# Kernel tuning notes

Measured on AMD Instinct MI355X. Metric: run time of the kernel, lower is better.

Reference implementation:

```python
import jax, jax.numpy as jnp
import numpy as np

XD, D, R, MIXN = 8, 64, 64, 32
BATCH, SEQ = 2048, 128
EPS = 1e-5
LOG2PI = float(np.log(2.0 * np.pi))


def softsign(x):
    return x / (1.0 + jnp.abs(x))


def batchnorm(x, gamma, beta):
    # BatchNorm1d in training mode: per-call batch statistics (biased var)
    mu = jnp.mean(x, axis=0)
    var = jnp.var(x, axis=0)
    return gamma * (x - mu) * jax.lax.rsqrt(var + EPS) + beta


def setup_inputs() -> dict:
    key = jax.random.key(0)
    ks = jax.random.split(key, 20)
    def lin(k, out_d, in_d):
        bound = 1.0 / np.sqrt(in_d)
        k1, k2 = jax.random.split(k)
        W = jax.random.uniform(k1, (out_d, in_d), minval=-bound, maxval=bound, dtype=jnp.float32)
        b = jax.random.uniform(k2, (out_d,), minval=-bound, maxval=bound, dtype=jnp.float32)
        return W, b
    X = jax.random.normal(ks[0], (BATCH, XD, SEQ), dtype=jnp.float32)
    enc_w, enc_b = lin(ks[1], D, XD)
    init_w = jax.random.normal(ks[2], (1, R), dtype=jnp.float32)
    A = jax.random.normal(ks[3], (R, D, R), dtype=jnp.float32)
    muW, mub = lin(ks[4], MIXN * XD, R)
    muW2, mub2 = lin(ks[5], MIXN * XD, MIXN * XD)
    sigW, sigb = lin(ks[6], MIXN * XD, R)
    sigW2, sigb2 = lin(ks[7], MIXN * XD, MIXN * XD)
    alW, alb = lin(ks[8], MIXN, R)
    alW2, alb2 = lin(ks[9], MIXN, MIXN)
    bn_g = jnp.ones((R,), jnp.float32)
    bn_b = jnp.zeros((R,), jnp.float32)
    return dict(X=X, enc_w=enc_w, enc_b=enc_b, init_w=init_w, A=A, bn_g=bn_g, bn_b=bn_b,
                muW=muW, mub=mub, muW2=muW2, mub2=mub2, sigW=sigW, sigb=sigb,
                sigW2=sigW2, sigb2=sigb2, alW=alW, alb=alb, alW2=alW2, alb2=alb2)


def reference(X, enc_w, enc_b, init_w, A, bn_g, bn_b,
              muW, mub, muW2, mub2, sigW, sigb, sigW2, sigb2,
              alW, alb, alW2, alb2):
    B, _, L = X.shape

    def phi(x, tmp):
        # GMM log-likelihood head; h = softmax of hidden state
        h = jax.nn.softmax(tmp, axis=1)                       # [B, R]
        mu = softsign(h @ muW.T + mub) @ muW2.T + mub2        # [B, MIXN*XD]
        logsig = softsign(h @ sigW.T + sigb) @ sigW2.T + sigb2
        log_alpha = jax.nn.log_softmax(
            softsign(h @ alW.T + alb) @ alW2.T + alb2, axis=1)  # [B, MIXN]
        mu = mu.reshape(B, MIXN, XD)
        logsig = logsig.reshape(B, MIXN, XD)
        sig = jnp.exp(logsig)
        z = (x[:, None, :] - mu) / sig
        comp_lp = jnp.sum(-0.5 * z * z - logsig - 0.5 * LOG2PI, axis=-1)  # [B, MIXN]
        return jax.scipy.special.logsumexp(log_alpha + comp_lp, axis=1)  # [B]

    # step 0: broadcast initial weight
    tmp0 = batchnorm(jnp.tile(init_w, (B, 1)), bn_g, bn_b)
    res0 = phi(X[:, :, 0], tmp0)
    norm0 = jnp.sum(tmp0 * tmp0)

    x_prev = jnp.moveaxis(X[:, :, :L - 1], 2, 0)  # [L-1, B, XD]
    x_cur = jnp.moveaxis(X[:, :, 1:], 2, 0)       # [L-1, B, XD]

    def step(carry, inputs):
        tmp, res, norm = carry
        xp, xc = inputs
        enc = softsign(xp @ enc_w.T + enc_b)                 # encoding()
        new = jnp.einsum('nd,ni,idj->nj', enc, tmp, A)       # trilinear transition
        new = batchnorm(new, bn_g, bn_b)
        res = res + phi(xc, new)
        norm = norm + jnp.sum(new * new)
        return (new, res, norm), None

    (_, res, norm), _ = jax.lax.scan(step, (tmp0, res0, norm0), (x_prev, x_cur))
    return res, norm
```

## Files before the change

### kernel.cpp

```cpp
#include <hip/hip_runtime.h>

typedef unsigned short u16;
typedef short short8 __attribute__((ext_vector_type(8)));
typedef float f32x4 __attribute__((ext_vector_type(4)));
typedef unsigned uint4v __attribute__((ext_vector_type(4)));

#define LOG2PI_HALF 0.91893853320467274f
#define AO __ATOMIC_RELAXED
#define AS __HIP_MEMORY_SCOPE_AGENT

static constexpr size_t OFF_STATS = 0;
static constexpr size_t OFF_NEW   = 65536;
static constexpr size_t OFF_AT    = OFF_NEW + (size_t)128*2048*64*2;
static constexpr size_t OFF_MUW   = OFF_AT   + (size_t)64*4096*2;
static constexpr size_t OFF_SIGW  = OFF_MUW  + (size_t)256*64*2;
static constexpr size_t OFF_ALW   = OFF_SIGW + (size_t)256*64*2;
static constexpr size_t OFF_MUW2  = OFF_ALW  + (size_t)32*64*2;
static constexpr size_t OFF_SIGW2 = OFF_MUW2 + (size_t)256*256*2;
static constexpr size_t OFF_ALW2  = OFF_SIGW2+ (size_t)256*256*2;
static constexpr size_t OFF_CNT   = OFF_ALW2 + (size_t)32*32*2;
static constexpr size_t OFF_PART  = OFF_CNT + 1024;
static constexpr size_t WS_NEED   = OFF_PART + (size_t)2*128*128*4;

static __device__ __forceinline__ u16 f2bf(float x) {
  unsigned u = __builtin_bit_cast(unsigned, x);
  u += 0x7fffu + ((u >> 16) & 1u);
  return (u16)(u >> 16);
}
static __device__ __forceinline__ float bf2f(u16 b) {
  unsigned u = ((unsigned)b) << 16;
  return __builtin_bit_cast(float, u);
}
static __device__ __forceinline__ unsigned pk2(float a, float b) {
  return ((unsigned)f2bf(b) << 16) | (unsigned)f2bf(a);
}

__global__ void init_kernel(
    const float* __restrict__ A, const float* __restrict__ init_w,
    const float* __restrict__ muW, const float* __restrict__ sigW, const float* __restrict__ alW,
    const float* __restrict__ muW2, const float* __restrict__ sigW2, const float* __restrict__ alW2,
    u16* __restrict__ At, u16* __restrict__ new0, float* __restrict__ stats0,
    u16* __restrict__ muWb, u16* __restrict__ sigWb, u16* __restrict__ alWb,
    u16* __restrict__ muW2b, u16* __restrict__ sigW2b, u16* __restrict__ alW2b)
{
  const int total = 560192;
  for (int idx = blockIdx.x*256 + threadIdx.x; idx < total; idx += gridDim.x*256) {
    if (idx < 262144) {
      int j = idx >> 12, k = idx & 4095;
      At[idx] = f2bf(A[k*64 + j]);
    } else if (idx < 393216) {
      int e = idx - 262144;
      new0[e] = f2bf(init_w[e & 63]);
    } else if (idx < 409600) { int e = idx - 393216; muWb[e]   = f2bf(muW[e]);
    } else if (idx < 425984) { int e = idx - 409600; sigWb[e]  = f2bf(sigW[e]);
    } else if (idx < 428032) { int e = idx - 425984; alWb[e]   = f2bf(alW[e]);
    } else if (idx < 493568) { int e = idx - 428032; muW2b[e]  = f2bf(muW2[e]);
    } else if (idx < 559104) { int e = idx - 493568; sigW2b[e] = f2bf(sigW2[e]);
    } else if (idx < 560128) { int e = idx - 559104; alW2b[e]  = f2bf(alW2[e]);
    } else {
      int e = idx - 560128;
      float wv = bf2f(f2bf(init_w[e]));
      stats0[e]      = 2048.0f * wv;
      stats0[64 + e] = 2048.0f * (wv * wv);
    }
  }
}

struct ChainS {
  float newf[16][64];
  float tmp_s[16][66];
  float enc_s[16][68];
  float xp_s[16][8];
  float ab_s[2][64];
  float psum[4][128];
  float red_s[8][16][64];
  float sred[2][16][66];
};
struct PhiS {
  u16 h_s[32][72];
  u16 smu[32][264];
  u16 ssg[32][264];
  u16 sal[32][40];
  float xc_s[32][8];
  float clp_s[32][32];
  float alo_s[32][34];
  float bias_s[1088];
  float ab2[2][64];
};
union SmemU { ChainS c; PhiS p; };

__global__ __launch_bounds__(512) void fused_kernel(
    u16* __restrict__ newa, float* stats, int* flags, float* part,
    const float* __restrict__ X,
    const float* __restrict__ enc_w, const float* __restrict__ enc_b,
    const float* __restrict__ bn_g, const float* __restrict__ bn_b,
    const u16* __restrict__ At, const float* __restrict__ init_w,
    const u16* __restrict__ muWb, const u16* __restrict__ sigWb, const u16* __restrict__ alWb,
    const u16* __restrict__ muW2b, const u16* __restrict__ sigW2b, const u16* __restrict__ alW2b,
    const float* __restrict__ mub, const float* __restrict__ sigb, const float* __restrict__ alb,
    const float* __restrict__ mub2, const float* __restrict__ sigb2, const float* __restrict__ alb2,
    float* __restrict__ outp)
{
  __shared__ SmemU smem;
  const int tid = threadIdx.x;
  const int bid = blockIdx.x;
  const int lane = tid & 63, w = tid >> 6;
  const int m = lane & 15, q = lane >> 4;
  int* sflag = flags + 128;

  if (bid < 128) {
    const int n0 = bid * 16;
    for (int e = tid; e < 1024; e += 512) {
      int r = e >> 6, c0 = e & 63;
      smem.c.newf[r][c0] = bf2f(f2bf(init_w[c0]));
    }

    for (int t = 1; t < 128; ++t) {
      if (tid < 128) {
        int r = tid >> 3, k = tid & 7;
        smem.c.xp_s[r][k] = X[(size_t)(n0+r)*1024 + k*128 + (t-1)];
      }
      __syncthreads();
      {
        int r = tid >> 5, d0 = (tid & 31) * 2;
        #pragma unroll
        for (int dd = 0; dd < 2; ++dd) {
          int d = d0 + dd;
          float a = enc_b[d];
          #pragma unroll
          for (int k = 0; k < 8; ++k) a = fmaf(smem.c.xp_s[r][k], enc_w[d*8+k], a);
          smem.c.enc_s[r][d] = a / (1.0f + fabsf(a));
        }
      }

      if (t >= 2) {
        if (w == 0) {
          for (;;) {
            int v0 = __hip_atomic_load(flags + lane*2,     AO, AS);
            int v1 = __hip_atomic_load(flags + lane*2 + 1, AO, AS);
            if (__ballot((v0 >= t-1) && (v1 >= t-1)) == ~0ull) break;
            __builtin_amdgcn_s_sleep(1);
          }
        }
        __syncthreads();
        __atomic_signal_fence(__ATOMIC_ACQUIRE);
        {
          const int e = tid & 127, pr = tid >> 7;
          const float* pb = part + (size_t)((t-1)&1)*16384 + e;
          float s = 0.0f;
          #pragma unroll 16
          for (int p = pr*32; p < pr*32 + 32; ++p)
            s += __hip_atomic_load(pb + p*128, AO, AS);
          smem.c.psum[pr][e] = s;
        }
        __syncthreads();
        if (bid == 0 && tid < 128) {
          float sv = smem.c.psum[0][tid] + smem.c.psum[1][tid] + smem.c.psum[2][tid] + smem.c.psum[3][tid];
          __hip_atomic_store(stats + (t-1)*128 + tid, sv, AO, AS);
        }
        if (tid < 64) {
          float S1 = smem.c.psum[0][tid] + smem.c.psum[1][tid] + smem.c.psum[2][tid] + smem.c.psum[3][tid];
          float S2 = smem.c.psum[0][tid+64] + smem.c.psum[1][tid+64] + smem.c.psum[2][tid+64] + smem.c.psum[3][tid+64];
          float mean = S1 * (1.0f/2048.0f);
          float var  = S2 * (1.0f/2048.0f) - mean*mean;
          float a = bn_g[tid] * rsqrtf(var + 1e-5f);
          smem.c.ab_s[0][tid] = a;
          smem.c.ab_s[1][tid] = fmaf(-a, mean, bn_b[tid]);
        }
      } else {
        if (tid < 64) {
          float mean = bf2f(f2bf(init_w[tid]));
          float a = bn_g[tid] * rsqrtf(1e-5f);
          smem.c.ab_s[0][tid] = a;
          smem.c.ab_s[1][tid] = fmaf(-a, mean, bn_b[tid]);
        }
      }
      __syncthreads();
      if (bid == 0 && tid == 0 && t >= 2)
        __hip_atomic_store(sflag, t-1, AO, AS);

      #pragma unroll
      for (int e0 = 0; e0 < 1024; e0 += 512) {
        int e = e0 + tid;
        int mr = e >> 6, i = e & 63;
        smem.c.tmp_s[mr][i] = fmaf(smem.c.ab_s[0][i], smem.c.newf[mr][i], smem.c.ab_s[1][i]);
      }
      __syncthreads();

      f32x4 acc[4];
      #pragma unroll
      for (int nt = 0; nt < 4; ++nt) acc[nt] = 0;

      #pragma unroll 4
      for (int it = 0; it < 16; ++it) {
        const int k0 = w*512 + it*32;
        const int i = k0 >> 6;
        const int dbase = (k0 & 63) + q*8;
        const float tv = smem.c.tmp_s[m][i];
        const f32x4 e0 = *reinterpret_cast<const f32x4*>(&smem.c.enc_s[m][dbase]);
        const f32x4 e1 = *reinterpret_cast<const f32x4*>(&smem.c.enc_s[m][dbase+4]);
        uint4v pk;
        pk[0] = pk2(tv*e0[0], tv*e0[1]);
        pk[1] = pk2(tv*e0[2], tv*e0[3]);
        pk[2] = pk2(tv*e1[0], tv*e1[1]);
        pk[3] = pk2(tv*e1[2], tv*e1[3]);
        short8 af = __builtin_bit_cast(short8, pk);
        const u16* bp = At + k0 + q*8;
        #pragma unroll
        for (int nt = 0; nt < 4; ++nt) {
          short8 bfv = *reinterpret_cast<const short8*>(bp + (nt*16 + m)*4096);
          acc[nt] = __builtin_amdgcn_mfma_f32_16x16x32_bf16(af, bfv, acc[nt], 0, 0, 0);
        }
      }
      #pragma unroll
      for (int nt = 0; nt < 4; ++nt)
        #pragma unroll
        for (int rg = 0; rg < 4; ++rg)
          smem.c.red_s[w][q*4+rg][nt*16+m] = acc[nt][rg];
      __syncthreads();

      {
        u16* no = newa + (size_t)t*2048*64;
        const int r = tid >> 5;
        const int c2 = (tid & 31) * 2;
        float v0 = 0.0f, v1 = 0.0f;
        #pragma unroll
        for (int p = 0; p < 8; ++p) { v0 += smem.c.red_s[p][r][c2]; v1 += smem.c.red_s[p][r][c2+1]; }
        smem.c.newf[r][c2]   = v0;
        smem.c.newf[r][c2+1] = v1;
        __hip_atomic_store((unsigned*)(no + (size_t)(n0+r)*64 + c2), pk2(v0, v1), AO, AS);
        smem.c.sred[0][r][c2]   = v0;  smem.c.sred[0][r][c2+1] = v1;
        smem.c.sred[1][r][c2]   = v0*v0; smem.c.sred[1][r][c2+1] = v1*v1;
      }
      __syncthreads();
      if (tid < 64) {
        float S1 = 0.0f, S2 = 0.0f;
        #pragma unroll
        for (int r = 0; r < 16; ++r) { S1 += smem.c.sred[0][r][tid]; S2 += smem.c.sred[1][r][tid]; }
        float* pb = part + (size_t)(t&1)*16384 + bid*128;
        __hip_atomic_store(pb + tid,      S1, AO, AS);
        __hip_atomic_store(pb + 64 + tid, S2, AO, AS);
      }
      __syncthreads();
      if (tid == 0)
        __hip_atomic_store(flags + bid, t, AO, AS);
    }

    if (bid == 0) {
      if (w == 0) {
        for (;;) {
          int v0 = __hip_atomic_load(flags + lane*2,     AO, AS);
          int v1 = __hip_atomic_load(flags + lane*2 + 1, AO, AS);
          if (__ballot((v0 >= 127) && (v1 >= 127)) == ~0ull) break;
          __builtin_amdgcn_s_sleep(1);
        }
      }
      __syncthreads();
      __atomic_signal_fence(__ATOMIC_ACQUIRE);
      {
        const int e = tid & 127, pr = tid >> 7;
        const float* pb = part + (size_t)(127&1)*16384 + e;
        float s = 0.0f;
        #pragma unroll 16
        for (int p = pr*32; p < pr*32 + 32; ++p)
          s += __hip_atomic_load(pb + p*128, AO, AS);
        smem.c.psum[pr][e] = s;
      }
      __syncthreads();
      if (tid < 128) {
        float sv = smem.c.psum[0][tid] + smem.c.psum[1][tid] + smem.c.psum[2][tid] + smem.c.psum[3][tid];
        __hip_atomic_store(stats + 127*128 + tid, sv, AO, AS);
      }
      __syncthreads();
      if (tid == 0) __hip_atomic_store(sflag, 127, AO, AS);
    }

  } else {
    const int cc  = bid - 128;
    const int n0p = (cc & 63) * 32;
    const int par = cc >> 6;
    const int r32 = tid >> 4;
    const int x16 = tid & 15;

    for (int e = tid; e < 1088; e += 512) {
      float v;
      if      (e < 256)  v = mub[e];
      else if (e < 512)  v = sigb[e-256];
      else if (e < 544)  v = alb[e-512];
      else if (e < 800)  v = mub2[e-544];
      else if (e < 1056) v = sigb2[e-800];
      else               v = alb2[e-1056];
      smem.p.bias_s[e] = v;
    }
    float nrm_acc = 0.0f;

    for (int kk = 0; kk < 64; ++kk) {
      const int t = 2*kk + par;
      if (t > 0 && tid == 0) {
        while (__hip_atomic_load(sflag, AO, AS) < t)
          __builtin_amdgcn_s_sleep(1);
      }
      __syncthreads();
      __atomic_signal_fence(__ATOMIC_ACQUIRE);
      if (tid < 64) {
        float s1 = __hip_atomic_load(stats + t*128 + tid,      AO, AS);
        float s2 = __hip_atomic_load(stats + t*128 + 64 + tid, AO, AS);
        float mean = s1 * (1.0f/2048.0f);
        float var  = s2 * (1.0f/2048.0f) - mean*mean;
        float a = bn_g[tid] * rsqrtf(var + 1e-5f);
        smem.p.ab2[0][tid] = a;
        smem.p.ab2[1][tid] = fmaf(-a, mean, bn_b[tid]);
      }
      __syncthreads();

      {
        const u16* na = newa + (size_t)t*2048*64 + (size_t)(n0p + r32)*64 + x16*4;
        unsigned d0 = __hip_atomic_load((const unsigned*)na,     AO, AS);
        unsigned d1 = __hip_atomic_load((const unsigned*)na + 1, AO, AS);
        const int ib = x16*4;
        float tv[4];
        tv[0] = fmaf(smem.p.ab2[0][ib],   bf2f((u16)(d0 & 0xffff)), smem.p.ab2[1][ib]);
        tv[1] = fmaf(smem.p.ab2[0][ib+1], bf2f((u16)(d0 >> 16)),    smem.p.ab2[1][ib+1]);
        tv[2] = fmaf(smem.p.ab2[0][ib+2], bf2f((u16)(d1 & 0xffff)), smem.p.ab2[1][ib+2]);
        tv[3] = fmaf(smem.p.ab2[0][ib+3], bf2f((u16)(d1 >> 16)),    smem.p.ab2[1][ib+3]);
        float nacc = 0.0f, mx = -3.4e38f;
        #pragma unroll
        for (int j = 0; j < 4; ++j) { nacc = fmaf(tv[j], tv[j], nacc); mx = fmaxf(mx, tv[j]); }
        mx = fmaxf(mx, __shfl_xor(mx, 1));
        mx = fmaxf(mx, __shfl_xor(mx, 2));
        mx = fmaxf(mx, __shfl_xor(mx, 4));
        mx = fmaxf(mx, __shfl_xor(mx, 8));
        float se = 0.0f;
        #pragma unroll
        for (int j = 0; j < 4; ++j) { tv[j] = __expf(tv[j] - mx); se += tv[j]; }
        se += __shfl_xor(se, 1);
        se += __shfl_xor(se, 2);
        se += __shfl_xor(se, 4);
        se += __shfl_xor(se, 8);
        float inv = 1.0f / se;
        #pragma unroll
        for (int j = 0; j < 4; ++j) smem.p.h_s[r32][ib + j] = f2bf(tv[j] * inv);
        nacc += __shfl_xor(nacc, 1);
        nacc += __shfl_xor(nacc, 2);
        nacc += __shfl_xor(nacc, 4);
        nacc += __shfl_xor(nacc, 8);
        nacc += __shfl_xor(nacc, 16);
        nacc += __shfl_xor(nacc, 32);
        nrm_acc += nacc;
        if (x16 < 8) smem.p.xc_s[r32][x16] = X[(size_t)(n0p+r32)*1024 + x16*128 + t];
      }
      __syncthreads();

      {
        const u16* W1 = (w < 4) ? muWb : sigWb;
        const int boff = (w < 4) ? 0 : 256;
        const int coloff = (w & 3) * 64;
        f32x4 acc2[2][4];
        #pragma unroll
        for (int a_ = 0; a_ < 2; ++a_)
          #pragma unroll
          for (int b_ = 0; b_ < 4; ++b_) acc2[a_][b_] = 0;
        #pragma unroll
        for (int mt = 0; mt < 2; ++mt)
          #pragma unroll
          for (int kit = 0; kit < 2; ++kit) {
            short8 af = *reinterpret_cast<const short8*>(&smem.p.h_s[mt*16+m][kit*32 + q*8]);
            #pragma unroll
            for (int nt = 0; nt < 4; ++nt) {
              int c_ = coloff + nt*16 + m;
              short8 bfv = *reinterpret_cast<const short8*>(W1 + c_*64 + kit*32 + q*8);
              acc2[mt][nt] = __builtin_amdgcn_mfma_f32_16x16x32_bf16(af, bfv, acc2[mt][nt], 0, 0, 0);
            }
          }
        #pragma unroll
        for (int mt = 0; mt < 2; ++mt)
          #pragma unroll
          for (int nt = 0; nt < 4; ++nt) {
            int col = coloff + nt*16 + m;
            float bia = smem.p.bias_s[boff + col];
            #pragma unroll
            for (int rg = 0; rg < 4; ++rg) {
              int row = mt*16 + q*4 + rg;
              float v = acc2[mt][nt][rg] + bia;
              v = v / (1.0f + fabsf(v));
              ((w < 4) ? smem.p.smu : smem.p.ssg)[row][col] = f2bf(v);
            }
          }
      }
      if (w == 0) {
        f32x4 aacc[2][2];
        aacc[0][0] = 0; aacc[0][1] = 0; aacc[1][0] = 0; aacc[1][1] = 0;
        #pragma unroll
        for (int mt = 0; mt < 2; ++mt)
          #pragma unroll
          for (int kit = 0; kit < 2; ++kit) {
            short8 af = *reinterpret_cast<const short8*>(&smem.p.h_s[mt*16+m][kit*32 + q*8]);
            #pragma unroll
            for (int nt = 0; nt < 2; ++nt) {
              short8 bfv = *reinterpret_cast<const short8*>(alWb + (nt*16+m)*64 + kit*32 + q*8);
              aacc[mt][nt] = __builtin_amdgcn_mfma_f32_16x16x32_bf16(af, bfv, aacc[mt][nt], 0, 0, 0);
            }
          }
        #pragma unroll
        for (int mt = 0; mt < 2; ++mt)
          #pragma unroll
          for (int nt = 0; nt < 2; ++nt) {
            int col = nt*16 + m;
            float bia = smem.p.bias_s[512 + col];
            #pragma unroll
            for (int rg = 0; rg < 4; ++rg) {
              int row = mt*16 + q*4 + rg;
              float v = aacc[mt][nt][rg] + bia;
              v = v / (1.0f + fabsf(v));
              smem.p.sal[row][col] = f2bf(v);
            }
          }
      }
      __syncthreads();

      {
        #pragma unroll 1
        for (int mt = 0; mt < 2; ++mt) {
          f32x4 accm[2], accs[2];
          accm[0] = 0; accm[1] = 0; accs[0] = 0; accs[1] = 0;
          for (int kit = 0; kit < 8; ++kit) {
            short8 am_ = *reinterpret_cast<const short8*>(&smem.p.smu[mt*16+m][kit*32 + q*8]);
            short8 as_ = *reinterpret_cast<const short8*>(&smem.p.ssg[mt*16+m][kit*32 + q*8]);
            #pragma unroll
            for (int nt = 0; nt < 2; ++nt) {
              int cb = w*32 + nt*16 + m;
              short8 bm = *reinterpret_cast<const short8*>(muW2b + cb*256 + kit*32 + q*8);
              short8 bs = *reinterpret_cast<const short8*>(sigW2b + cb*256 + kit*32 + q*8);
              accm[nt] = __builtin_amdgcn_mfma_f32_16x16x32_bf16(am_, bm, accm[nt], 0, 0, 0);
              accs[nt] = __builtin_amdgcn_mfma_f32_16x16x32_bf16(as_, bs, accs[nt], 0, 0, 0);
            }
          }
          #pragma unroll
          for (int nt = 0; nt < 2; ++nt) {
            int col = w*32 + nt*16 + m;
            int cmix = col >> 3, x = col & 7;
            float bmu = smem.p.bias_s[544 + col], bsg = smem.p.bias_s[800 + col];
            #pragma unroll
            for (int rg = 0; rg < 4; ++rg) {
              int row = mt*16 + q*4 + rg;
              float muv = accm[nt][rg] + bmu;
              float lsv = accs[nt][rg] + bsg;
              float z = (smem.p.xc_s[row][x] - muv) * __expf(-lsv);
              float tt = fmaf(-0.5f*z, z, -lsv) - LOG2PI_HALF;
              tt += __shfl_xor(tt, 1);
              tt += __shfl_xor(tt, 2);
              tt += __shfl_xor(tt, 4);
              if (x == 0) smem.p.clp_s[row][cmix] = tt;
            }
          }
        }
        if (w == 0) {
          #pragma unroll
          for (int mt = 0; mt < 2; ++mt) {
            f32x4 aacc[2]; aacc[0] = 0; aacc[1] = 0;
            short8 aa = *reinterpret_cast<const short8*>(&smem.p.sal[mt*16+m][q*8]);
            #pragma unroll
            for (int nt = 0; nt < 2; ++nt) {
              short8 bb = *reinterpret_cast<const short8*>(alW2b + (nt*16+m)*32 + q*8);
              aacc[nt] = __builtin_amdgcn_mfma_f32_16x16x32_bf16(aa, bb, aacc[nt], 0, 0, 0);
            }
            #pragma unroll
            for (int nt = 0; nt < 2; ++nt) {
              int col = nt*16 + m;
              float bia = smem.p.bias_s[1056 + col];
              #pragma unroll
              for (int rg = 0; rg < 4; ++rg)
                smem.p.alo_s[mt*16 + q*4 + rg][col] = aacc[nt][rg] + bia;
            }
          }
        }
      }
      __syncthreads();

      {
        const int r = r32, jj = x16;
        float av[2], am = -3.4e38f;
        #pragma unroll
        for (int u = 0; u < 2; ++u) { av[u] = smem.p.alo_s[r][jj + u*16]; am = fmaxf(am, av[u]); }
        am = fmaxf(am, __shfl_xor(am, 1));
        am = fmaxf(am, __shfl_xor(am, 2));
        am = fmaxf(am, __shfl_xor(am, 4));
        am = fmaxf(am, __shfl_xor(am, 8));
        float se = 0.0f;
        #pragma unroll
        for (int u = 0; u < 2; ++u) se += __expf(av[u] - am);
        se += __shfl_xor(se, 1);
        se += __shfl_xor(se, 2);
        se += __shfl_xor(se, 4);
        se += __shfl_xor(se, 8);
        float la = am + __logf(se);
        float tt2[2], tm = -3.4e38f;
        #pragma unroll
        for (int u = 0; u < 2; ++u) {
          tt2[u] = av[u] - la + smem.p.clp_s[r][jj + u*16];
          tm = fmaxf(tm, tt2[u]);
        }
        tm = fmaxf(tm, __shfl_xor(tm, 1));
        tm = fmaxf(tm, __shfl_xor(tm, 2));
        tm = fmaxf(tm, __shfl_xor(tm, 4));
        tm = fmaxf(tm, __shfl_xor(tm, 8));
        float ts = 0.0f;
        #pragma unroll
        for (int u = 0; u < 2; ++u) ts += __expf(tt2[u] - tm);
        ts += __shfl_xor(ts, 1);
        ts += __shfl_xor(ts, 2);
        ts += __shfl_xor(ts, 4);
        ts += __shfl_xor(ts, 8);
        if (jj == 0) atomicAdd(&outp[n0p + r], tm + __logf(ts));
      }
      __syncthreads();
    }
    if (lane == 0) atomicAdd(&outp[2048], nrm_acc);
  }
}

extern "C" void kernel_launch(void* const* d_in, const int* in_sizes, int n_in,
                              void* d_out, int out_size, void* d_ws, size_t ws_size,
                              hipStream_t stream) {
  const float* X      = (const float*)d_in[0];
  const float* enc_w  = (const float*)d_in[1];
  const float* enc_b  = (const float*)d_in[2];
  const float* init_w = (const float*)d_in[3];
  const float* A      = (const float*)d_in[4];
  const float* bn_g   = (const float*)d_in[5];
  const float* bn_b   = (const float*)d_in[6];
  const float* muW    = (const float*)d_in[7];
  const float* mub    = (const float*)d_in[8];
  const float* muW2   = (const float*)d_in[9];
  const float* mub2   = (const float*)d_in[10];
  const float* sigW   = (const float*)d_in[11];
  const float* sigb   = (const float*)d_in[12];
  const float* sigW2  = (const float*)d_in[13];
  const float* sigb2  = (const float*)d_in[14];
  const float* alW    = (const float*)d_in[15];
  const float* alb    = (const float*)d_in[16];
  const float* alW2   = (const float*)d_in[17];
  const float* alb2   = (const float*)d_in[18];

  if (ws_size < WS_NEED) return;

  char* ws = (char*)d_ws;
  float* stats = (float*)(ws + OFF_STATS);
  u16* newa    = (u16*)(ws + OFF_NEW);
  u16* At      = (u16*)(ws + OFF_AT);
  u16* muWb    = (u16*)(ws + OFF_MUW);
  u16* sigWb   = (u16*)(ws + OFF_SIGW);
  u16* alWb    = (u16*)(ws + OFF_ALW);
  u16* muW2b   = (u16*)(ws + OFF_MUW2);
  u16* sigW2b  = (u16*)(ws + OFF_SIGW2);
  u16* alW2b   = (u16*)(ws + OFF_ALW2);
  int* flags   = (int*)(ws + OFF_CNT);
  float* part  = (float*)(ws + OFF_PART);

  (void)hipMemsetAsync(d_out, 0, (size_t)out_size * sizeof(float), stream);
  (void)hipMemsetAsync(stats, 0, (size_t)128 * 128 * sizeof(float), stream);
  (void)hipMemsetAsync(flags, 0, 1024, stream);

  init_kernel<<<dim3(1024), dim3(256), 0, stream>>>(
      A, init_w, muW, sigW, alW, muW2, sigW2, alW2,
      At, newa, stats, muWb, sigWb, alWb, muW2b, sigW2b, alW2b);

  {
    u16* newa_a = newa; float* stats_a = stats; int* flags_a = flags; float* part_a = part;
    const float *X_a = X, *encw_a = enc_w, *encb_a = enc_b, *bng_a = bn_g, *bnb_a = bn_b, *initw_a = init_w;
    const u16 *At_a = At, *muWb_a = muWb, *sigWb_a = sigWb, *alWb_a = alWb,
              *muW2b_a = muW2b, *sigW2b_a = sigW2b, *alW2b_a = alW2b;
    const float *mub_a = mub, *sigb_a = sigb, *alb_a = alb, *mub2_a = mub2, *sigb2_a = sigb2, *alb2_a = alb2;
    float* outp_a = (float*)d_out;
    void* args[] = { (void*)&newa_a, (void*)&stats_a, (void*)&flags_a, (void*)&part_a, (void*)&X_a,
                     (void*)&encw_a, (void*)&encb_a, (void*)&bng_a, (void*)&bnb_a, (void*)&At_a, (void*)&initw_a,
                     (void*)&muWb_a, (void*)&sigWb_a, (void*)&alWb_a,
                     (void*)&muW2b_a, (void*)&sigW2b_a, (void*)&alW2b_a,
                     (void*)&mub_a, (void*)&sigb_a, (void*)&alb_a,
                     (void*)&mub2_a, (void*)&sigb2_a, (void*)&alb2_a,
                     (void*)&outp_a };
    (void)hipLaunchCooperativeKernel((void*)fused_kernel, dim3(256), dim3(512), args, 0, stream);
  }
}
```

Measured before the change: 2.377 ms.

## Halve chain blocks to 32 rows each and split phi work three ways

The recurrent chain now runs on 64 blocks of 32 rows instead of 128 blocks of 16 rows. Each wave handles 16 rows and a quarter of the K dimension, and the normalised state is computed in registers instead of a separate shared tmp buffer with an extra barrier. The phi consumer blocks now cover timesteps with stride 3 instead of 2 parity halves, so more blocks run the GMM head in parallel. The aim is to cut the grid-wide flag polling and partial-sum reduction cost on every step, at the cost of more serial MFMA work per chain block on the critical path.

```diff
diff --git a/kernel.cpp b/kernel.cpp
--- a/kernel.cpp
+++ b/kernel.cpp
@@ -1,6 +1,7 @@
 #include <hip/hip_runtime.h>
 
 typedef unsigned short u16;
+typedef unsigned long long u64;
 typedef short short8 __attribute__((ext_vector_type(8)));
 typedef float f32x4 __attribute__((ext_vector_type(4)));
 typedef unsigned uint4v __attribute__((ext_vector_type(4)));
@@ -20,7 +21,7 @@
 static constexpr size_t OFF_ALW2  = OFF_SIGW2+ (size_t)256*256*2;
 static constexpr size_t OFF_CNT   = OFF_ALW2 + (size_t)32*32*2;
 static constexpr size_t OFF_PART  = OFF_CNT + 1024;
-static constexpr size_t WS_NEED   = OFF_PART + (size_t)2*128*128*4;
+static constexpr size_t WS_NEED   = OFF_PART + (size_t)2*64*128*4;
 
 static __device__ __forceinline__ u16 f2bf(float x) {
   unsigned u = __builtin_bit_cast(unsigned, x);
@@ -67,14 +68,12 @@
 }
 
 struct ChainS {
-  float newf[16][64];
-  float tmp_s[16][66];
-  float enc_s[16][68];
-  float xp_s[16][8];
+  float newf[32][66];
+  float enc_s[32][68];
+  float xp_s[32][8];
   float ab_s[2][64];
   float psum[4][128];
-  float red_s[8][16][64];
-  float sred[2][16][66];
+  float red[8][16][66];
 };
 struct PhiS {
   u16 h_s[32][72];
@@ -108,23 +107,26 @@
   const int m = lane & 15, q = lane >> 4;
   int* sflag = flags + 128;
 
-  if (bid < 128) {
-    const int n0 = bid * 16;
-    for (int e = tid; e < 1024; e += 512) {
+  if (bid < 64) {
+    const int n0 = bid * 32;
+    const int tl = w >> 2, kq = w & 3;
+    const int row = tl*16 + m;
+
+    for (int e = tid; e < 2048; e += 512) {
       int r = e >> 6, c0 = e & 63;
       smem.c.newf[r][c0] = bf2f(f2bf(init_w[c0]));
     }
 
     for (int t = 1; t < 128; ++t) {
-      if (tid < 128) {
+      if (tid < 256) {
         int r = tid >> 3, k = tid & 7;
         smem.c.xp_s[r][k] = X[(size_t)(n0+r)*1024 + k*128 + (t-1)];
       }
       __syncthreads();
       {
-        int r = tid >> 5, d0 = (tid & 31) * 2;
-        #pragma unroll
-        for (int dd = 0; dd < 2; ++dd) {
+        int r = tid >> 4, d0 = (tid & 15) * 4;
+        #pragma unroll
+        for (int dd = 0; dd < 4; ++dd) {
           int d = d0 + dd;
           float a = enc_b[d];
           #pragma unroll
@@ -136,9 +138,8 @@
       if (t >= 2) {
         if (w == 0) {
           for (;;) {
-            int v0 = __hip_atomic_load(flags + lane*2,     AO, AS);
-            int v1 = __hip_atomic_load(flags + lane*2 + 1, AO, AS);
-            if (__ballot((v0 >= t-1) && (v1 >= t-1)) == ~0ull) break;
+            int v = __hip_atomic_load(flags + lane, AO, AS);
+            if (__ballot(v >= t-1) == ~0ull) break;
             __builtin_amdgcn_s_sleep(1);
           }
         }
@@ -146,10 +147,10 @@
         __atomic_signal_fence(__ATOMIC_ACQUIRE);
         {
           const int e = tid & 127, pr = tid >> 7;
-          const float* pb = part + (size_t)((t-1)&1)*16384 + e;
+          const float* pb = part + (size_t)((t-1)&1)*8192 + e;
           float s = 0.0f;
           #pragma unroll 16
-          for (int p = pr*32; p < pr*32 + 32; ++p)
+          for (int p = pr*16; p < pr*16 + 16; ++p)
             s += __hip_atomic_load(pb + p*128, AO, AS);
           smem.c.psum[pr][e] = s;
         }
@@ -179,31 +180,29 @@
       if (bid == 0 && tid == 0 && t >= 2)
         __hip_atomic_store(sflag, t-1, AO, AS);
 
+      float tv[16];
       #pragma unroll
-      for (int e0 = 0; e0 < 1024; e0 += 512) {
-        int e = e0 + tid;
-        int mr = e >> 6, i = e & 63;
-        smem.c.tmp_s[mr][i] = fmaf(smem.c.ab_s[0][i], smem.c.newf[mr][i], smem.c.ab_s[1][i]);
-      }
-      __syncthreads();
+      for (int ii = 0; ii < 16; ++ii) {
+        int i = kq*16 + ii;
+        tv[ii] = fmaf(smem.c.ab_s[0][i], smem.c.newf[row][i], smem.c.ab_s[1][i]);
+      }
 
       f32x4 acc[4];
       #pragma unroll
       for (int nt = 0; nt < 4; ++nt) acc[nt] = 0;
 
       #pragma unroll 4
-      for (int it = 0; it < 16; ++it) {
-        const int k0 = w*512 + it*32;
-        const int i = k0 >> 6;
-        const int dbase = (k0 & 63) + q*8;
-        const float tv = smem.c.tmp_s[m][i];
-        const f32x4 e0 = *reinterpret_cast<const f32x4*>(&smem.c.enc_s[m][dbase]);
-        const f32x4 e1 = *reinterpret_cast<const f32x4*>(&smem.c.enc_s[m][dbase+4]);
+      for (int it = 0; it < 32; ++it) {
+        const int k0 = kq*1024 + it*32;
+        const int dbase = ((it & 1) << 5) + q*8;
+        const float tvv = tv[it >> 1];
+        const f32x4 e0 = *reinterpret_cast<const f32x4*>(&smem.c.enc_s[row][dbase]);
+        const f32x4 e1 = *reinterpret_cast<const f32x4*>(&smem.c.enc_s[row][dbase+4]);
         uint4v pk;
-        pk[0] = pk2(tv*e0[0], tv*e0[1]);
-        pk[1] = pk2(tv*e0[2], tv*e0[3]);
-        pk[2] = pk2(tv*e1[0], tv*e1[1]);
-        pk[3] = pk2(tv*e1[2], tv*e1[3]);
+        pk[0] = pk2(tvv*e0[0], tvv*e0[1]);
+        pk[1] = pk2(tvv*e0[2], tvv*e0[3]);
+        pk[2] = pk2(tvv*e1[0], tvv*e1[1]);
+        pk[3] = pk2(tvv*e1[2], tvv*e1[3]);
         short8 af = __builtin_bit_cast(short8, pk);
         const u16* bp = At + k0 + q*8;
         #pragma unroll
@@ -216,28 +215,35 @@
       for (int nt = 0; nt < 4; ++nt)
         #pragma unroll
         for (int rg = 0; rg < 4; ++rg)
-          smem.c.red_s[w][q*4+rg][nt*16+m] = acc[nt][rg];
+          smem.c.red[w][q*4+rg][nt*16+m] = acc[nt][rg];
       __syncthreads();
 
       {
         u16* no = newa + (size_t)t*2048*64;
-        const int r = tid >> 5;
-        const int c2 = (tid & 31) * 2;
-        float v0 = 0.0f, v1 = 0.0f;
-        #pragma unroll
-        for (int p = 0; p < 8; ++p) { v0 += smem.c.red_s[p][r][c2]; v1 += smem.c.red_s[p][r][c2+1]; }
-        smem.c.newf[r][c2]   = v0;
-        smem.c.newf[r][c2+1] = v1;
-        __hip_atomic_store((unsigned*)(no + (size_t)(n0+r)*64 + c2), pk2(v0, v1), AO, AS);
-        smem.c.sred[0][r][c2]   = v0;  smem.c.sred[0][r][c2+1] = v1;
-        smem.c.sred[1][r][c2]   = v0*v0; smem.c.sred[1][r][c2+1] = v1*v1;
+        const int r = tid >> 4;
+        const int c0 = (tid & 15) * 4;
+        const int tl2 = r >> 4, rr = r & 15;
+        float v[4];
+        #pragma unroll
+        for (int j = 0; j < 4; ++j) {
+          float s = 0.0f;
+          #pragma unroll
+          for (int kk = 0; kk < 4; ++kk) s += smem.c.red[tl2*4+kk][rr][c0+j];
+          v[j] = s;
+          smem.c.newf[r][c0+j] = s;
+        }
+        u64 pv = ((u64)pk2(v[2], v[3]) << 32) | (u64)pk2(v[0], v[1]);
+        __hip_atomic_store((u64*)(no + (size_t)(n0+r)*64 + c0), pv, AO, AS);
       }
       __syncthreads();
       if (tid < 64) {
         float S1 = 0.0f, S2 = 0.0f;
         #pragma unroll
-        for (int r = 0; r < 16; ++r) { S1 += smem.c.sred[0][r][tid]; S2 += smem.c.sred[1][r][tid]; }
-        float* pb = part + (size_t)(t&1)*16384 + bid*128;
+        for (int r = 0; r < 32; ++r) {
+          float vv = smem.c.newf[r][tid];
+          S1 += vv; S2 = fmaf(vv, vv, S2);
+        }
+        float* pb = part + (size_t)(t&1)*8192 + bid*128;
         __hip_atomic_store(pb + tid,      S1, AO, AS);
         __hip_atomic_store(pb + 64 + tid, S2, AO, AS);
       }
@@ -249,9 +255,8 @@
     if (bid == 0) {
       if (w == 0) {
         for (;;) {
-          int v0 = __hip_atomic_load(flags + lane*2,     AO, AS);
-          int v1 = __hip_atomic_load(flags + lane*2 + 1, AO, AS);
-          if (__ballot((v0 >= 127) && (v1 >= 127)) == ~0ull) break;
+          int v = __hip_atomic_load(flags + lane, AO, AS);
+          if (__ballot(v >= 127) == ~0ull) break;
           __builtin_amdgcn_s_sleep(1);
         }
       }
@@ -259,10 +264,10 @@
       __atomic_signal_fence(__ATOMIC_ACQUIRE);
       {
         const int e = tid & 127, pr = tid >> 7;
-        const float* pb = part + (size_t)(127&1)*16384 + e;
+        const float* pb = part + (size_t)8192 + e;
         float s = 0.0f;
         #pragma unroll 16
-        for (int p = pr*32; p < pr*32 + 32; ++p)
+        for (int p = pr*16; p < pr*16 + 16; ++p)
           s += __hip_atomic_load(pb + p*128, AO, AS);
         smem.c.psum[pr][e] = s;
       }
@@ -276,9 +281,9 @@
     }
 
   } else {
-    const int cc  = bid - 128;
+    const int cc  = bid - 64;
     const int n0p = (cc & 63) * 32;
-    const int par = cc >> 6;
+    const int ph  = cc >> 6;
     const int r32 = tid >> 4;
     const int x16 = tid & 15;
 
@@ -294,8 +299,7 @@
     }
     float nrm_acc = 0.0f;
 
-    for (int kk = 0; kk < 64; ++kk) {
-      const int t = 2*kk + par;
+    for (int t = ph; t < 128; t += 3) {
       if (t > 0 && tid == 0) {
         while (__hip_atomic_load(sflag, AO, AS) < t)
           __builtin_amdgcn_s_sleep(1);
@@ -318,28 +322,28 @@
         unsigned d0 = __hip_atomic_load((const unsigned*)na,     AO, AS);
         unsigned d1 = __hip_atomic_load((const unsigned*)na + 1, AO, AS);
         const int ib = x16*4;
-        float tv[4];
-        tv[0] = fmaf(smem.p.ab2[0][ib],   bf2f((u16)(d0 & 0xffff)), smem.p.ab2[1][ib]);
-        tv[1] = fmaf(smem.p.ab2[0][ib+1], bf2f((u16)(d0 >> 16)),    smem.p.ab2[1][ib+1]);
-        tv[2] = fmaf(smem.p.ab2[0][ib+2], bf2f((u16)(d1 & 0xffff)), smem.p.ab2[1][ib+2]);
-        tv[3] = fmaf(smem.p.ab2[0][ib+3], bf2f((u16)(d1 >> 16)),    smem.p.ab2[1][ib+3]);
+        float tvv[4];
+        tvv[0] = fmaf(smem.p.ab2[0][ib],   bf2f((u16)(d0 & 0xffff)), smem.p.ab2[1][ib]);
+        tvv[1] = fmaf(smem.p.ab2[0][ib+1], bf2f((u16)(d0 >> 16)),    smem.p.ab2[1][ib+1]);
+        tvv[2] = fmaf(smem.p.ab2[0][ib+2], bf2f((u16)(d1 & 0xffff)), smem.p.ab2[1][ib+2]);
+        tvv[3] = fmaf(smem.p.ab2[0][ib+3], bf2f((u16)(d1 >> 16)),    smem.p.ab2[1][ib+3]);
         float nacc = 0.0f, mx = -3.4e38f;
         #pragma unroll
-        for (int j = 0; j < 4; ++j) { nacc = fmaf(tv[j], tv[j], nacc); mx = fmaxf(mx, tv[j]); }
+        for (int j = 0; j < 4; ++j) { nacc = fmaf(tvv[j], tvv[j], nacc); mx = fmaxf(mx, tvv[j]); }
         mx = fmaxf(mx, __shfl_xor(mx, 1));
         mx = fmaxf(mx, __shfl_xor(mx, 2));
         mx = fmaxf(mx, __shfl_xor(mx, 4));
         mx = fmaxf(mx, __shfl_xor(mx, 8));
         float se = 0.0f;
         #pragma unroll
-        for (int j = 0; j < 4; ++j) { tv[j] = __expf(tv[j] - mx); se += tv[j]; }
+        for (int j = 0; j < 4; ++j) { tvv[j] = __expf(tvv[j] - mx); se += tvv[j]; }
         se += __shfl_xor(se, 1);
         se += __shfl_xor(se, 2);
         se += __shfl_xor(se, 4);
         se += __shfl_xor(se, 8);
         float inv = 1.0f / se;
         #pragma unroll
-        for (int j = 0; j < 4; ++j) smem.p.h_s[r32][ib + j] = f2bf(tv[j] * inv);
+        for (int j = 0; j < 4; ++j) smem.p.h_s[r32][ib + j] = f2bf(tvv[j] * inv);
         nacc += __shfl_xor(nacc, 1);
         nacc += __shfl_xor(nacc, 2);
         nacc += __shfl_xor(nacc, 4);
@@ -380,10 +384,10 @@
             float bia = smem.p.bias_s[boff + col];
             #pragma unroll
             for (int rg = 0; rg < 4; ++rg) {
-              int row = mt*16 + q*4 + rg;
+              int rw = mt*16 + q*4 + rg;
               float v = acc2[mt][nt][rg] + bia;
               v = v / (1.0f + fabsf(v));
-              ((w < 4) ? smem.p.smu : smem.p.ssg)[row][col] = f2bf(v);
+              ((w < 4) ? smem.p.smu : smem.p.ssg)[rw][col] = f2bf(v);
             }
           }
       }
@@ -409,10 +413,10 @@
             float bia = smem.p.bias_s[512 + col];
             #pragma unroll
             for (int rg = 0; rg < 4; ++rg) {
-              int row = mt*16 + q*4 + rg;
+              int rw = mt*16 + q*4 + rg;
               float v = aacc[mt][nt][rg] + bia;
               v = v / (1.0f + fabsf(v));
-              smem.p.sal[row][col] = f2bf(v);
+              smem.p.sal[rw][col] = f2bf(v);
             }
           }
       }
@@ -442,15 +446,15 @@
             float bmu = smem.p.bias_s[544 + col], bsg = smem.p.bias_s[800 + col];
             #pragma unroll
             for (int rg = 0; rg < 4; ++rg) {
-              int row = mt*16 + q*4 + rg;
+              int rw = mt*16 + q*4 + rg;
               float muv = accm[nt][rg] + bmu;
               float lsv = accs[nt][rg] + bsg;
-              float z = (smem.p.xc_s[row][x] - muv) * __expf(-lsv);
+              float z = (smem.p.xc_s[rw][x] - muv) * __expf(-lsv);
               float tt = fmaf(-0.5f*z, z, -lsv) - LOG2PI_HALF;
               tt += __shfl_xor(tt, 1);
               tt += __shfl_xor(tt, 2);
               tt += __shfl_xor(tt, 4);
-              if (x == 0) smem.p.clp_s[row][cmix] = tt;
+              if (x == 0) smem.p.clp_s[rw][cmix] = tt;
             }
           }
         }
```

New measurement: 4.126 ms. 1.74x slower.

## Centralize per-step batchnorm reduction in a dedicated block and rebalance phi work

Applied to the files above, without the earlier changes.

Each chain block used to poll all 128 progress flags and reduce every block's partial sums itself. Now one dedicated block (bid 128) does that reduction and publishes the batchnorm scale/shift per step to a global array behind a single flag, which chain and phi blocks wait on. The phi blocks drop the even/odd step split and stride over all (step, 32-row tile) work items, and the partial-sum buffer is no longer double-buffered. The aim is to cut redundant global reads and polling traffic on every chain block, at the cost of an extra signalling hop on the serial step critical path.

```diff
diff --git a/kernel.cpp b/kernel.cpp
--- a/kernel.cpp
+++ b/kernel.cpp
@@ -9,7 +9,7 @@
 #define AO __ATOMIC_RELAXED
 #define AS __HIP_MEMORY_SCOPE_AGENT
 
-static constexpr size_t OFF_STATS = 0;
+static constexpr size_t OFF_ABG   = 0;
 static constexpr size_t OFF_NEW   = 65536;
 static constexpr size_t OFF_AT    = OFF_NEW + (size_t)128*2048*64*2;
 static constexpr size_t OFF_MUW   = OFF_AT   + (size_t)64*4096*2;
@@ -20,7 +20,7 @@
 static constexpr size_t OFF_ALW2  = OFF_SIGW2+ (size_t)256*256*2;
 static constexpr size_t OFF_CNT   = OFF_ALW2 + (size_t)32*32*2;
 static constexpr size_t OFF_PART  = OFF_CNT + 1024;
-static constexpr size_t WS_NEED   = OFF_PART + (size_t)2*128*128*4;
+static constexpr size_t WS_NEED   = OFF_PART + (size_t)128*128*4;
 
 static __device__ __forceinline__ u16 f2bf(float x) {
   unsigned u = __builtin_bit_cast(unsigned, x);
@@ -39,11 +39,11 @@
     const float* __restrict__ A, const float* __restrict__ init_w,
     const float* __restrict__ muW, const float* __restrict__ sigW, const float* __restrict__ alW,
     const float* __restrict__ muW2, const float* __restrict__ sigW2, const float* __restrict__ alW2,
-    u16* __restrict__ At, u16* __restrict__ new0, float* __restrict__ stats0,
+    u16* __restrict__ At, u16* __restrict__ new0,
     u16* __restrict__ muWb, u16* __restrict__ sigWb, u16* __restrict__ alWb,
     u16* __restrict__ muW2b, u16* __restrict__ sigW2b, u16* __restrict__ alW2b)
 {
-  const int total = 560192;
+  const int total = 560128;
   for (int idx = blockIdx.x*256 + threadIdx.x; idx < total; idx += gridDim.x*256) {
     if (idx < 262144) {
       int j = idx >> 12, k = idx & 4095;
@@ -56,12 +56,7 @@
     } else if (idx < 428032) { int e = idx - 425984; alWb[e]   = f2bf(alW[e]);
     } else if (idx < 493568) { int e = idx - 428032; muW2b[e]  = f2bf(muW2[e]);
     } else if (idx < 559104) { int e = idx - 493568; sigW2b[e] = f2bf(sigW2[e]);
-    } else if (idx < 560128) { int e = idx - 559104; alW2b[e]  = f2bf(alW2[e]);
-    } else {
-      int e = idx - 560128;
-      float wv = bf2f(f2bf(init_w[e]));
-      stats0[e]      = 2048.0f * wv;
-      stats0[64 + e] = 2048.0f * (wv * wv);
+    } else                   { int e = idx - 559104; alW2b[e]  = f2bf(alW2[e]);
     }
   }
 }
@@ -90,7 +85,7 @@
 union SmemU { ChainS c; PhiS p; };
 
 __global__ __launch_bounds__(512) void fused_kernel(
-    u16* __restrict__ newa, float* stats, int* flags, float* part,
+    u16* __restrict__ newa, float* ab_g, int* flags, float* part,
     const float* __restrict__ X,
     const float* __restrict__ enc_w, const float* __restrict__ enc_b,
     const float* __restrict__ bn_g, const float* __restrict__ bn_b,
@@ -132,52 +127,17 @@
           smem.c.enc_s[r][d] = a / (1.0f + fabsf(a));
         }
       }
-
-      if (t >= 2) {
-        if (w == 0) {
-          for (;;) {
-            int v0 = __hip_atomic_load(flags + lane*2,     AO, AS);
-            int v1 = __hip_atomic_load(flags + lane*2 + 1, AO, AS);
-            if (__ballot((v0 >= t-1) && (v1 >= t-1)) == ~0ull) break;
-            __builtin_amdgcn_s_sleep(1);
-          }
-        }
-        __syncthreads();
-        __atomic_signal_fence(__ATOMIC_ACQUIRE);
-        {
-          const int e = tid & 127, pr = tid >> 7;
-          const float* pb = part + (size_t)((t-1)&1)*16384 + e;
-          float s = 0.0f;
-          #pragma unroll 16
-          for (int p = pr*32; p < pr*32 + 32; ++p)
-            s += __hip_atomic_load(pb + p*128, AO, AS);
-          smem.c.psum[pr][e] = s;
-        }
-        __syncthreads();
-        if (bid == 0 && tid < 128) {
-          float sv = smem.c.psum[0][tid] + smem.c.psum[1][tid] + smem.c.psum[2][tid] + smem.c.psum[3][tid];
-          __hip_atomic_store(stats + (t-1)*128 + tid, sv, AO, AS);
-        }
-        if (tid < 64) {
-          float S1 = smem.c.psum[0][tid] + smem.c.psum[1][tid] + smem.c.psum[2][tid] + smem.c.psum[3][tid];
-          float S2 = smem.c.psum[0][tid+64] + smem.c.psum[1][tid+64] + smem.c.psum[2][tid+64] + smem.c.psum[3][tid+64];
-          float mean = S1 * (1.0f/2048.0f);
-          float var  = S2 * (1.0f/2048.0f) - mean*mean;
-          float a = bn_g[tid] * rsqrtf(var + 1e-5f);
-          smem.c.ab_s[0][tid] = a;
-          smem.c.ab_s[1][tid] = fmaf(-a, mean, bn_b[tid]);
-        }
-      } else {
-        if (tid < 64) {
-          float mean = bf2f(f2bf(init_w[tid]));
-          float a = bn_g[tid] * rsqrtf(1e-5f);
-          smem.c.ab_s[0][tid] = a;
-          smem.c.ab_s[1][tid] = fmaf(-a, mean, bn_b[tid]);
-        }
-      }
-      __syncthreads();
-      if (bid == 0 && tid == 0 && t >= 2)
-        __hip_atomic_store(sflag, t-1, AO, AS);
+      if (tid == 0) {
+        while (__hip_atomic_load(sflag, AO, AS) < t)
+          __builtin_amdgcn_s_sleep(1);
+      }
+      __syncthreads();
+      __atomic_signal_fence(__ATOMIC_ACQUIRE);
+      if (tid < 64) {
+        smem.c.ab_s[0][tid] = __hip_atomic_load(ab_g + (t-1)*128 + tid,      AO, AS);
+        smem.c.ab_s[1][tid] = __hip_atomic_load(ab_g + (t-1)*128 + 64 + tid, AO, AS);
+      }
+      __syncthreads();
 
       #pragma unroll
       for (int e0 = 0; e0 < 1024; e0 += 512) {
@@ -229,7 +189,7 @@
         smem.c.newf[r][c2]   = v0;
         smem.c.newf[r][c2+1] = v1;
         __hip_atomic_store((unsigned*)(no + (size_t)(n0+r)*64 + c2), pk2(v0, v1), AO, AS);
-        smem.c.sred[0][r][c2]   = v0;  smem.c.sred[0][r][c2+1] = v1;
+        smem.c.sred[0][r][c2]   = v0;    smem.c.sred[0][r][c2+1] = v1;
         smem.c.sred[1][r][c2]   = v0*v0; smem.c.sred[1][r][c2+1] = v1*v1;
       }
       __syncthreads();
@@ -237,7 +197,7 @@
         float S1 = 0.0f, S2 = 0.0f;
         #pragma unroll
         for (int r = 0; r < 16; ++r) { S1 += smem.c.sred[0][r][tid]; S2 += smem.c.sred[1][r][tid]; }
-        float* pb = part + (size_t)(t&1)*16384 + bid*128;
+        float* pb = part + (size_t)bid*128;
         __hip_atomic_store(pb + tid,      S1, AO, AS);
         __hip_atomic_store(pb + 64 + tid, S2, AO, AS);
       }
@@ -246,12 +206,22 @@
         __hip_atomic_store(flags + bid, t, AO, AS);
     }
 
-    if (bid == 0) {
+  } else if (bid == 128) {
+    if (tid < 64) {
+      float wv = bf2f(f2bf(init_w[tid]));
+      float a = bn_g[tid] * rsqrtf(1e-5f);
+      __hip_atomic_store(ab_g + tid,      a,                        AO, AS);
+      __hip_atomic_store(ab_g + 64 + tid, fmaf(-a, wv, bn_b[tid]), AO, AS);
+    }
+    __syncthreads();
+    if (tid == 0) __hip_atomic_store(sflag, 1, AO, AS);
+
+    for (int t = 1; t < 128; ++t) {
       if (w == 0) {
         for (;;) {
           int v0 = __hip_atomic_load(flags + lane*2,     AO, AS);
           int v1 = __hip_atomic_load(flags + lane*2 + 1, AO, AS);
-          if (__ballot((v0 >= 127) && (v1 >= 127)) == ~0ull) break;
+          if (__ballot((v0 >= t) && (v1 >= t)) == ~0ull) break;
           __builtin_amdgcn_s_sleep(1);
         }
       }
@@ -259,7 +229,7 @@
       __atomic_signal_fence(__ATOMIC_ACQUIRE);
       {
         const int e = tid & 127, pr = tid >> 7;
-        const float* pb = part + (size_t)(127&1)*16384 + e;
+        const float* pb = part + e;
         float s = 0.0f;
         #pragma unroll 16
         for (int p = pr*32; p < pr*32 + 32; ++p)
@@ -267,18 +237,21 @@
         smem.c.psum[pr][e] = s;
       }
       __syncthreads();
-      if (tid < 128) {
-        float sv = smem.c.psum[0][tid] + smem.c.psum[1][tid] + smem.c.psum[2][tid] + smem.c.psum[3][tid];
-        __hip_atomic_store(stats + 127*128 + tid, sv, AO, AS);
-      }
-      __syncthreads();
-      if (tid == 0) __hip_atomic_store(sflag, 127, AO, AS);
+      if (tid < 64) {
+        float S1 = smem.c.psum[0][tid] + smem.c.psum[1][tid] + smem.c.psum[2][tid] + smem.c.psum[3][tid];
+        float S2 = smem.c.psum[0][tid+64] + smem.c.psum[1][tid+64] + smem.c.psum[2][tid+64] + smem.c.psum[3][tid+64];
+        float mean = S1 * (1.0f/2048.0f);
+        float var  = S2 * (1.0f/2048.0f) - mean*mean;
+        float a = bn_g[tid] * rsqrtf(var + 1e-5f);
+        __hip_atomic_store(ab_g + t*128 + tid,      a,                          AO, AS);
+        __hip_atomic_store(ab_g + t*128 + 64 + tid, fmaf(-a, mean, bn_b[tid]), AO, AS);
+      }
+      __syncthreads();
+      if (tid == 0) __hip_atomic_store(sflag, t+1, AO, AS);
     }
 
   } else {
-    const int cc  = bid - 128;
-    const int n0p = (cc & 63) * 32;
-    const int par = cc >> 6;
+    const int cc  = bid - 129;
     const int r32 = tid >> 4;
     const int x16 = tid & 15;
 
@@ -294,22 +267,18 @@
     }
     float nrm_acc = 0.0f;
 
-    for (int kk = 0; kk < 64; ++kk) {
-      const int t = 2*kk + par;
-      if (t > 0 && tid == 0) {
-        while (__hip_atomic_load(sflag, AO, AS) < t)
+    for (int u = cc; u < 8192; u += 127) {
+      const int t   = u >> 6;
+      const int n0p = (u & 63) * 32;
+      if (tid == 0) {
+        while (__hip_atomic_load(sflag, AO, AS) < t+1)
           __builtin_amdgcn_s_sleep(1);
       }
       __syncthreads();
       __atomic_signal_fence(__ATOMIC_ACQUIRE);
       if (tid < 64) {
-        float s1 = __hip_atomic_load(stats + t*128 + tid,      AO, AS);
-        float s2 = __hip_atomic_load(stats + t*128 + 64 + tid, AO, AS);
-        float mean = s1 * (1.0f/2048.0f);
-        float var  = s2 * (1.0f/2048.0f) - mean*mean;
-        float a = bn_g[tid] * rsqrtf(var + 1e-5f);
-        smem.p.ab2[0][tid] = a;
-        smem.p.ab2[1][tid] = fmaf(-a, mean, bn_b[tid]);
+        smem.p.ab2[0][tid] = __hip_atomic_load(ab_g + t*128 + tid,      AO, AS);
+        smem.p.ab2[1][tid] = __hip_atomic_load(ab_g + t*128 + 64 + tid, AO, AS);
       }
       __syncthreads();
 
@@ -318,28 +287,28 @@
         unsigned d0 = __hip_atomic_load((const unsigned*)na,     AO, AS);
         unsigned d1 = __hip_atomic_load((const unsigned*)na + 1, AO, AS);
         const int ib = x16*4;
-        float tv[4];
-        tv[0] = fmaf(smem.p.ab2[0][ib],   bf2f((u16)(d0 & 0xffff)), smem.p.ab2[1][ib]);
-        tv[1] = fmaf(smem.p.ab2[0][ib+1], bf2f((u16)(d0 >> 16)),    smem.p.ab2[1][ib+1]);
-        tv[2] = fmaf(smem.p.ab2[0][ib+2], bf2f((u16)(d1 & 0xffff)), smem.p.ab2[1][ib+2]);
-        tv[3] = fmaf(smem.p.ab2[0][ib+3], bf2f((u16)(d1 >> 16)),    smem.p.ab2[1][ib+3]);
+        float tvv[4];
+        tvv[0] = fmaf(smem.p.ab2[0][ib],   bf2f((u16)(d0 & 0xffff)), smem.p.ab2[1][ib]);
+        tvv[1] = fmaf(smem.p.ab2[0][ib+1], bf2f((u16)(d0 >> 16)),    smem.p.ab2[1][ib+1]);
+        tvv[2] = fmaf(smem.p.ab2[0][ib+2], bf2f((u16)(d1 & 0xffff)), smem.p.ab2[1][ib+2]);
+        tvv[3] = fmaf(smem.p.ab2[0][ib+3], bf2f((u16)(d1 >> 16)),    smem.p.ab2[1][ib+3]);
         float nacc = 0.0f, mx = -3.4e38f;
         #pragma unroll
-        for (int j = 0; j < 4; ++j) { nacc = fmaf(tv[j], tv[j], nacc); mx = fmaxf(mx, tv[j]); }
+        for (int j = 0; j < 4; ++j) { nacc = fmaf(tvv[j], tvv[j], nacc); mx = fmaxf(mx, tvv[j]); }
         mx = fmaxf(mx, __shfl_xor(mx, 1));
         mx = fmaxf(mx, __shfl_xor(mx, 2));
         mx = fmaxf(mx, __shfl_xor(mx, 4));
         mx = fmaxf(mx, __shfl_xor(mx, 8));
         float se = 0.0f;
         #pragma unroll
-        for (int j = 0; j < 4; ++j) { tv[j] = __expf(tv[j] - mx); se += tv[j]; }
+        for (int j = 0; j < 4; ++j) { tvv[j] = __expf(tvv[j] - mx); se += tvv[j]; }
         se += __shfl_xor(se, 1);
         se += __shfl_xor(se, 2);
         se += __shfl_xor(se, 4);
         se += __shfl_xor(se, 8);
         float inv = 1.0f / se;
         #pragma unroll
-        for (int j = 0; j < 4; ++j) smem.p.h_s[r32][ib + j] = f2bf(tv[j] * inv);
+        for (int j = 0; j < 4; ++j) smem.p.h_s[r32][ib + j] = f2bf(tvv[j] * inv);
         nacc += __shfl_xor(nacc, 1);
         nacc += __shfl_xor(nacc, 2);
         nacc += __shfl_xor(nacc, 4);
@@ -380,10 +349,10 @@
             float bia = smem.p.bias_s[boff + col];
             #pragma unroll
             for (int rg = 0; rg < 4; ++rg) {
-              int row = mt*16 + q*4 + rg;
+              int rw = mt*16 + q*4 + rg;
               float v = acc2[mt][nt][rg] + bia;
               v = v / (1.0f + fabsf(v));
-              ((w < 4) ? smem.p.smu : smem.p.ssg)[row][col] = f2bf(v);
+              ((w < 4) ? smem.p.smu : smem.p.ssg)[rw][col] = f2bf(v);
             }
           }
       }
@@ -409,10 +378,10 @@
             float bia = smem.p.bias_s[512 + col];
             #pragma unroll
             for (int rg = 0; rg < 4; ++rg) {
-              int row = mt*16 + q*4 + rg;
+              int rw = mt*16 + q*4 + rg;
               float v = aacc[mt][nt][rg] + bia;
               v = v / (1.0f + fabsf(v));
-              smem.p.sal[row][col] = f2bf(v);
+              smem.p.sal[rw][col] = f2bf(v);
             }
           }
       }
@@ -442,15 +411,15 @@
             float bmu = smem.p.bias_s[544 + col], bsg = smem.p.bias_s[800 + col];
             #pragma unroll
             for (int rg = 0; rg < 4; ++rg) {
-              int row = mt*16 + q*4 + rg;
+              int rw = mt*16 + q*4 + rg;
               float muv = accm[nt][rg] + bmu;
               float lsv = accs[nt][rg] + bsg;
-              float z = (smem.p.xc_s[row][x] - muv) * __expf(-lsv);
+              float z = (smem.p.xc_s[rw][x] - muv) * __expf(-lsv);
               float tt = fmaf(-0.5f*z, z, -lsv) - LOG2PI_HALF;
               tt += __shfl_xor(tt, 1);
               tt += __shfl_xor(tt, 2);
               tt += __shfl_xor(tt, 4);
-              if (x == 0) smem.p.clp_s[row][cmix] = tt;
+              if (x == 0) smem.p.clp_s[rw][cmix] = tt;
             }
           }
         }
@@ -481,14 +450,14 @@
         const int r = r32, jj = x16;
         float av[2], am = -3.4e38f;
         #pragma unroll
-        for (int u = 0; u < 2; ++u) { av[u] = smem.p.alo_s[r][jj + u*16]; am = fmaxf(am, av[u]); }
+        for (int u2 = 0; u2 < 2; ++u2) { av[u2] = smem.p.alo_s[r][jj + u2*16]; am = fmaxf(am, av[u2]); }
         am = fmaxf(am, __shfl_xor(am, 1));
         am = fmaxf(am, __shfl_xor(am, 2));
         am = fmaxf(am, __shfl_xor(am, 4));
         am = fmaxf(am, __shfl_xor(am, 8));
         float se = 0.0f;
         #pragma unroll
-        for (int u = 0; u < 2; ++u) se += __expf(av[u] - am);
+        for (int u2 = 0; u2 < 2; ++u2) se += __expf(av[u2] - am);
         se += __shfl_xor(se, 1);
         se += __shfl_xor(se, 2);
         se += __shfl_xor(se, 4);
@@ -496,9 +465,9 @@
         float la = am + __logf(se);
         float tt2[2], tm = -3.4e38f;
         #pragma unroll
-        for (int u = 0; u < 2; ++u) {
-          tt2[u] = av[u] - la + smem.p.clp_s[r][jj + u*16];
-          tm = fmaxf(tm, tt2[u]);
+        for (int u2 = 0; u2 < 2; ++u2) {
+          tt2[u2] = av[u2] - la + smem.p.clp_s[r][jj + u2*16];
+          tm = fmaxf(tm, tt2[u2]);
         }
         tm = fmaxf(tm, __shfl_xor(tm, 1));
         tm = fmaxf(tm, __shfl_xor(tm, 2));
@@ -506,7 +475,7 @@
         tm = fmaxf(tm, __shfl_xor(tm, 8));
         float ts = 0.0f;
         #pragma unroll
-        for (int u = 0; u < 2; ++u) ts += __expf(tt2[u] - tm);
+        for (int u2 = 0; u2 < 2; ++u2) ts += __expf(tt2[u2] - tm);
         ts += __shfl_xor(ts, 1);
         ts += __shfl_xor(ts, 2);
         ts += __shfl_xor(ts, 4);
@@ -545,7 +514,7 @@
   if (ws_size < WS_NEED) return;
 
   char* ws = (char*)d_ws;
-  float* stats = (float*)(ws + OFF_STATS);
+  float* ab_g  = (float*)(ws + OFF_ABG);
   u16* newa    = (u16*)(ws + OFF_NEW);
   u16* At      = (u16*)(ws + OFF_AT);
   u16* muWb    = (u16*)(ws + OFF_MUW);
@@ -558,21 +527,20 @@
   float* part  = (float*)(ws + OFF_PART);
 
   (void)hipMemsetAsync(d_out, 0, (size_t)out_size * sizeof(float), stream);
-  (void)hipMemsetAsync(stats, 0, (size_t)128 * 128 * sizeof(float), stream);
   (void)hipMemsetAsync(flags, 0, 1024, stream);
 
   init_kernel<<<dim3(1024), dim3(256), 0, stream>>>(
       A, init_w, muW, sigW, alW, muW2, sigW2, alW2,
-      At, newa, stats, muWb, sigWb, alWb, muW2b, sigW2b, alW2b);
+      At, newa, muWb, sigWb, alWb, muW2b, sigW2b, alW2b);
 
   {
-    u16* newa_a = newa; float* stats_a = stats; int* flags_a = flags; float* part_a = part;
+    u16* newa_a = newa; float* abg_a = ab_g; int* flags_a = flags; float* part_a = part;
     const float *X_a = X, *encw_a = enc_w, *encb_a = enc_b, *bng_a = bn_g, *bnb_a = bn_b, *initw_a = init_w;
     const u16 *At_a = At, *muWb_a = muWb, *sigWb_a = sigWb, *alWb_a = alWb,
               *muW2b_a = muW2b, *sigW2b_a = sigW2b, *alW2b_a = alW2b;
     const float *mub_a = mub, *sigb_a = sigb, *alb_a = alb, *mub2_a = mub2, *sigb2_a = sigb2, *alb2_a = alb2;
     float* outp_a = (float*)d_out;
-    void* args[] = { (void*)&newa_a, (void*)&stats_a, (void*)&flags_a, (void*)&part_a, (void*)&X_a,
+    void* args[] = { (void*)&newa_a, (void*)&abg_a, (void*)&flags_a, (void*)&part_a, (void*)&X_a,
                      (void*)&encw_a, (void*)&encb_a, (void*)&bng_a, (void*)&bnb_a, (void*)&At_a, (void*)&initw_a,
                      (void*)&muWb_a, (void*)&sigWb_a, (void*)&alWb_a,
                      (void*)&muW2b_a, (void*)&sigW2b_a, (void*)&alW2b_a,
```

New measurement: 2.531 ms. 6.5% more time.
